# Kernel tuning notes

Measured on AMD Instinct MI355X. Metric: run time of the kernel, lower is better.

The kernel has to match this reference:

```python
import jax, jax.numpy as jnp
import numpy as np

B, N, P, T = 64, 200, 400, 1200
TOPK, STRIDE = 3, 25
THRESHOLD = 0.3  # args.threshold
EPS = 1e-9


def setup_inputs() -> dict:
    key = jax.random.key(0)
    k1, k2, k3 = jax.random.split(key, 3)
    x = jax.random.normal(k1, (B, N, T), jnp.float32)
    # xavier_uniform with gain=1.414 on (P, N) parameter
    limit = 1.414 * np.sqrt(6.0 / (P + N))
    patterns = jax.random.uniform(k2, (P, N), jnp.float32, -limit, limit)
    length = jax.random.randint(k3, (B,), 500, T + 1).astype(jnp.int32)
    return {"x": x, "patterns": patterns, "length": length}


def _forward(x, patterns, length):
    # size after temporal max-pool, per sample
    size_after_pool = jnp.floor(length.astype(jnp.float32) / STRIDE)  # (B,)

    # L2-normalize the learned patterns (P, N)
    normalized_patterns = patterns / jnp.sqrt((patterns ** 2).sum(-1, keepdims=True) + EPS)

    # top_select: keep top-K entries by |value| along node dim
    _, topi = jax.lax.top_k(jnp.abs(normalized_patterns), TOPK)  # (P, K)
    mask = jnp.zeros((P, N), jnp.float32).at[jnp.arange(P)[:, None], topi].set(1.0)
    toppattern = mask * normalized_patterns  # (P, N)

    # HCP_static branch: frames = x.transpose(2,1) -> (B, T, N)
    frames = x.transpose(0, 2, 1)
    normalized_frames = frames / jnp.sqrt((frames ** 2).sum(-1, keepdims=True) + EPS)

    # cosine similarity of every frame to every pattern: (B, T, P)
    sim = jnp.einsum('btn,pn->btp', normalized_frames, normalized_patterns)

    # non-overlapping max-pool over time with kernel=stride=STRIDE
    simw = sim.transpose(0, 2, 1).reshape(B, P, T // STRIDE, STRIDE)  # (B,P,Tp,S)
    posscores = simw.max(-1)          # (B, P, Tp)
    negscores = (-simw).max(-1)       # (B, P, Tp)
    sap = size_after_pool[:, None, None]
    compos = (posscores / sap).sum(-1)  # (B, P)
    comneg = (negscores / sap).sum(-1)  # (B, P)
    PES = (compos + comneg) / 2.0       # (B, P)

    # graphs = key_patterns.T @ diag(PES) @ key_patterns * non_diag_scale
    key_patterns = jax.lax.stop_gradient(toppattern)  # detach
    c = TOPK * P / N
    non_diag_scale = jnp.full((N, N), c, jnp.float32) - jnp.eye(N, dtype=jnp.float32) * (c - 1.0)
    graphs = jnp.einsum('pn,bp,pm->bnm', key_patterns, PES, key_patterns) * non_diag_scale

    # SigLoss(normalized_patterns, toppattern)
    lenp = jnp.linalg.norm(normalized_patterns, axis=-1)
    lentopp = jnp.linalg.norm(toppattern, axis=-1)
    norm = ((1.0 - lentopp / lenp) ** 2).mean()

    # Relaxed_orthloss(normalized_patterns, threshold)
    simpp = (normalized_patterns @ normalized_patterns.T) * (1.0 - jnp.eye(P, dtype=jnp.float32))
    orth = (jax.nn.relu((jnp.abs(simpp) - THRESHOLD) / (1.0 - THRESHOLD + 1e-5)) ** 2).mean()

    return graphs, norm, orth


def reference(x, patterns, length):
    return _forward(x, patterns, length)
```

## Files before the change

### kernel.cpp

```cpp
#include <hip/hip_runtime.h>
#include <math.h>

#define B_ 64
#define N_ 200
#define P_ 400
#define T_ 1200
#define TPAD 1280
#define PPAD 512
#define STRIDE_ 25
#define EPS_ 1e-9f
#define KPAD 224
#define BSTRIDE 232

#define OFF_NPATT  0
#define OFF_NPB16  80000
#define OFF_KEYVAL 124800
#define OFF_KEYIDX 126400
#define OFF_PES    128000
#define OFF_NORMB  153600
#define OFF_ORTHB  153700
#define OFF_NORM   OFF_NORMB
#define OFF_ORTH   OFF_ORTHB
#define OFF_NPBT   153728
#define OFF_XN     211072
#define OFF_GPOOL  9386112
#define WS_FAST_FLOATS (9386112 + 2457600)

#define ZO_BLKS  160
#define ZG_BLKS  40
#define ZP_BLKS  2
#define PAT_BLKS 100
#define TN_BLKS  (20 * B_)
#define Z_ALL    (ZO_BLKS + ZG_BLKS + ZP_BLKS)
#define PREP_BLKS (Z_ALL + PAT_BLKS + TN_BLKS)

typedef float f4v __attribute__((ext_vector_type(4)));
typedef short s8v __attribute__((ext_vector_type(8)));

__device__ inline unsigned short f2bf(float f) {
    union { float f; unsigned u; } v; v.f = f;
    unsigned r = v.u + 0x7FFFu + ((v.u >> 16) & 1u);
    return (unsigned short)(r >> 16);
}
__device__ inline unsigned okey(float f) {
    unsigned u = __float_as_uint(f);
    return (u & 0x80000000u) ? ~u : (u | 0x80000000u);
}
__device__ inline float dekey(unsigned k) {
    unsigned u = (k & 0x80000000u) ? (k & 0x7fffffffu) : ~k;
    return __uint_as_float(u);
}

__device__ float pat_body(const float* __restrict__ patterns, float* __restrict__ ws,
                          int p, int lane) {
    float v0 = patterns[p * N_ + lane];
    float v1 = patterns[p * N_ + lane + 64];
    float v2 = patterns[p * N_ + lane + 128];
    float v3 = (lane < 8) ? patterns[p * N_ + lane + 192] : 0.0f;

    float ss = v0 * v0 + v1 * v1 + v2 * v2 + v3 * v3;
    for (int off = 32; off; off >>= 1) ss += __shfl_down(ss, off);
    ss = __shfl(ss, 0);

    float rn = 1.0f / sqrtf(ss + EPS_);
    float s0 = v0 * rn, s1 = v1 * rn, s2 = v2 * rn, s3 = v3 * rn;

    float* npatT = ws + OFF_NPATT;
    npatT[(lane) * P_ + p] = s0;
    npatT[(lane + 64) * P_ + p] = s1;
    npatT[(lane + 128) * P_ + p] = s2;
    if (lane < 8) npatT[(lane + 192) * P_ + p] = s3;

    unsigned short* npb = (unsigned short*)(ws + OFF_NPB16);
    unsigned short b0 = f2bf(s0), b1 = f2bf(s1), b2 = f2bf(s2), b3 = f2bf(s3);
    npb[p * KPAD + lane] = b0;
    npb[p * KPAD + lane + 64] = b1;
    npb[p * KPAD + lane + 128] = b2;
    if (lane < 8) npb[p * KPAD + lane + 192] = b3;
    if (lane < 24) npb[p * KPAD + 200 + lane] = 0;

    unsigned short* npbT = (unsigned short*)(ws + OFF_NPBT);
    {
        int k0 = lane, k1 = lane + 64, k2 = lane + 128;
        npbT[(k0 >> 3) * (PPAD * 8) + p * 8 + (k0 & 7)] = b0;
        npbT[(k1 >> 3) * (PPAD * 8) + p * 8 + (k1 & 7)] = b1;
        npbT[(k2 >> 3) * (PPAD * 8) + p * 8 + (k2 & 7)] = b2;
        if (lane < 8) {
            int k3 = lane + 192;
            npbT[(k3 >> 3) * (PPAD * 8) + p * 8 + (k3 & 7)] = b3;
        }
        if (lane < 24) {
            int k4 = 200 + lane;
            npbT[(k4 >> 3) * (PPAD * 8) + p * 8 + (k4 & 7)] = 0;
        }
    }

    float a0 = fabsf(s0), a1 = fabsf(s1), a2 = fabsf(s2), a3 = fabsf(s3);

    int ch0 = -1, ch1 = -1, ch2 = -1;
    float cs0 = 0.f, cs1 = 0.f, cs2 = 0.f;

    for (int r = 0; r < 3; r++) {
        float bv = -1.0f;
        int bi = 1 << 30;
        {
            int n = lane;
            bool sk = (n == ch0) || (n == ch1) || (n == ch2);
            if (!sk && a0 > bv) { bv = a0; bi = n; }
        }
        {
            int n = lane + 64;
            bool sk = (n == ch0) || (n == ch1) || (n == ch2);
            if (!sk && (a1 > bv || (a1 == bv && n < bi))) { bv = a1; bi = n; }
        }
        {
            int n = lane + 128;
            bool sk = (n == ch0) || (n == ch1) || (n == ch2);
            if (!sk && (a2 > bv || (a2 == bv && n < bi))) { bv = a2; bi = n; }
        }
        if (lane < 8) {
            int n = lane + 192;
            bool sk = (n == ch0) || (n == ch1) || (n == ch2);
            if (!sk && (a3 > bv || (a3 == bv && n < bi))) { bv = a3; bi = n; }
        }
        for (int off = 32; off; off >>= 1) {
            float ov = __shfl_down(bv, off);
            int oi = __shfl_down(bi, off);
            if (ov > bv || (ov == bv && oi < bi)) { bv = ov; bi = oi; }
        }
        bi = __shfl(bi, 0);
        int slot = bi >> 6, src = bi & 63;
        float mine = (slot == 0) ? s0 : (slot == 1) ? s1 : (slot == 2) ? s2 : s3;
        float sval = __shfl(mine, src);
        if (r == 0) { ch0 = bi; cs0 = sval; }
        else if (r == 1) { ch1 = bi; cs1 = sval; }
        else { ch2 = bi; cs2 = sval; }
    }

    float d2 = 0.f;
    if (lane == 0) {
        float* keyval = ws + OFF_KEYVAL;
        int* keyidx = (int*)(ws + OFF_KEYIDX);
        keyval[p * 4 + 0] = cs0; keyval[p * 4 + 1] = cs1; keyval[p * 4 + 2] = cs2;
        keyidx[p * 4 + 0] = ch0; keyidx[p * 4 + 1] = ch1; keyidx[p * 4 + 2] = ch2;
        float lenp = sqrtf(ss) * rn;
        float lentopp = sqrtf(cs0 * cs0 + cs1 * cs1 + cs2 * cs2);
        float d = 1.0f - lentopp / lenp;
        d2 = d * d * (1.0f / (float)P_);
    }
    return d2;
}

__global__ __launch_bounds__(256) void prep_kernel(const float* __restrict__ x,
                                                   const float* __restrict__ patterns,
                                                   float* __restrict__ ws,
                                                   float* __restrict__ out) {
    __shared__ unsigned short xt16[64 * 210];
    __shared__ float psums[256];
    __shared__ float rns[64];
    __shared__ float sh4[4];

    const int tid = threadIdx.x;

    if (blockIdx.x < Z_ALL) {
        int zb = blockIdx.x;
        if (zb < ZO_BLKS) {
            uint4* o4 = (uint4*)out;
            for (int i = zb * 256 + tid; i < 640000; i += ZO_BLKS * 256)
                o4[i] = make_uint4(0, 0, 0, 0);
        } else if (zb < ZO_BLKS + ZG_BLKS) {
            uint4* gp4 = (uint4*)(ws + OFF_GPOOL);
            int base = (zb - ZO_BLKS) * 15360 + tid;
#pragma unroll
            for (int i = 0; i < 60; ++i)
                gp4[base + i * 256] = make_uint4(0, 0, 0, 0);
        } else {
            unsigned* p32 = (unsigned*)(ws + OFF_NPBT);
            int lb = zb - ZO_BLKS - ZG_BLKS;
            for (int e = lb * 256 + tid; e < 12544; e += ZP_BLKS * 256) {
                int seg = e / 448, r32 = e % 448;
                p32[seg * 2048 + 1600 + r32] = 0u;
            }
        }
        return;
    }

    if (blockIdx.x < Z_ALL + PAT_BLKS) {
        int pblk = blockIdx.x - Z_ALL;
        int wv = tid >> 6, lane = tid & 63;
        int p = pblk * 4 + wv;
        float d2 = pat_body(patterns, ws, p, lane);
        if (lane == 0) sh4[wv] = d2;
        __syncthreads();
        if (tid == 0)
            ws[OFF_NORMB + pblk] = sh4[0] + sh4[1] + sh4[2] + sh4[3];
        return;
    }

    const int blk = blockIdx.x - Z_ALL - PAT_BLKS;
    const int t = tid & 63, r = tid >> 6;
    const int b = blk / 20;
    const int t0 = (blk % 20) * 64;
    const bool valid = (t0 + t) < T_;

    float ss = 0.0f;
    if (valid) {
        const float* xp = x + (size_t)b * N_ * T_ + t0 + t;
#pragma unroll 5
        for (int i = 0; i < 50; ++i) {
            int n = r * 50 + i;
            float v = xp[(size_t)n * T_];
            ss += v * v;
            xt16[t * 210 + n] = f2bf(v);
        }
    }
    psums[tid] = ss;
    __syncthreads();
    if (tid < 64) {
        float s = psums[tid] + psums[tid + 64] + psums[tid + 128] + psums[tid + 192];
        rns[tid] = rsqrtf(s + EPS_);
    }
    __syncthreads();

    unsigned short* xnT = (unsigned short*)(ws + OFF_XN);
#pragma unroll
    for (int j = 0; j < 7; ++j) {
        int idx = tid + 256 * j;
        int seg = idx >> 6, tt = idx & 63;
        s8v ov = (s8v){0, 0, 0, 0, 0, 0, 0, 0};
        if (seg < 25 && (t0 + tt) < T_) {
            float rn = rns[tt];
            const unsigned* src = (const unsigned*)&xt16[tt * 210 + seg * 8];
            unsigned o[4];
#pragma unroll
            for (int i = 0; i < 4; ++i) {
                unsigned u = src[i];
                float lo = __uint_as_float(u << 16) * rn;
                float hi = __uint_as_float(u & 0xffff0000u) * rn;
                o[i] = (unsigned)f2bf(lo) | ((unsigned)f2bf(hi) << 16);
            }
            ov = (s8v){(short)(o[0] & 0xffff), (short)(o[0] >> 16),
                       (short)(o[1] & 0xffff), (short)(o[1] >> 16),
                       (short)(o[2] & 0xffff), (short)(o[2] >> 16),
                       (short)(o[3] & 0xffff), (short)(o[3] >> 16)};
        }
        *(s8v*)(xnT + (((size_t)b * 28 + seg) * TPAD + t0 + tt) * 8) = ov;
    }
}

__global__ __launch_bounds__(256, 4) void work_kernel(float* __restrict__ ws,
                                                      unsigned* __restrict__ gpool) {
    __shared__ short ldsB[80 * BSTRIDE];
    __shared__ unsigned pool[2 * 7 * 80];

    const int tid = threadIdx.x;
    int orig = blockIdx.x;
    int xcd = orig & 7, rem = orig >> 3;
    int nid = (xcd < 4 ? xcd * 83 : 4 * 83 + (xcd - 4) * 82) + rem;

    const bool isOrth = (nid >= 640);
    int pb, mbg, b;
    if (isOrth) { int o = nid - 640; pb = o % 5; mbg = o / 5; b = 0; }
    else        { pb = nid % 5; mbg = (nid / 5) % 2; b = nid / 10; }

    const unsigned short* npb = (const unsigned short*)(ws + OFF_NPB16) + (size_t)(pb * 80) * KPAD;

#pragma unroll
    for (int j = 0; j < 9; ++j) {
        int idx = tid + 256 * j;
        if (idx < 2240) {
            int row = idx / 28, seg = idx % 28;
            *(s8v*)(&ldsB[row * BSTRIDE + seg * 8]) = *(const s8v*)(npb + (size_t)row * KPAD + seg * 8);
        }
    }
    for (int i = tid; i < 1120; i += 256) pool[i] = 0u;
    __syncthreads();

    const int wv = tid >> 6;
    const int lane = tid & 63;
    const int l15 = lane & 15, kg = lane >> 4;

    const int ROWS = isOrth ? PPAD : TPAD;
    const unsigned short* abase = isOrth
        ? (const unsigned short*)(ws + OFF_NPBT)
        : (const unsigned short*)(ws + OFF_XN) + (size_t)b * 28 * TPAD * 8;
    const int segstep = 4 * ROWS * 8;
    const int niter = isOrth ? 1 : 5;

    float orthpart = 0.f;

    for (int it = 0; it < niter; ++it) {
        const int mb = isOrth ? mbg : (mbg * 5 + it);
        const int row0 = mb * 128 + wv * 32 + l15;
        const unsigned short* ar0 = abase + ((size_t)kg * ROWS + row0) * 8;
        const unsigned short* ar1 = ar0 + 16 * 8;

        f4v acc[2][5];
#pragma unroll
        for (int mi = 0; mi < 2; ++mi)
#pragma unroll
            for (int ni = 0; ni < 5; ++ni) acc[mi][ni] = (f4v){0.f, 0.f, 0.f, 0.f};

        s8v A[4][2];
#pragma unroll
        for (int c = 0; c < 4; ++c) {
            A[c][0] = *(const s8v*)(ar0 + c * segstep);
            A[c][1] = *(const s8v*)(ar1 + c * segstep);
        }

#pragma unroll
        for (int c = 0; c < 7; ++c) {
            if (c + 4 < 7) {
                A[(c + 4) & 3][0] = *(const s8v*)(ar0 + (c + 4) * segstep);
                A[(c + 4) & 3][1] = *(const s8v*)(ar1 + (c + 4) * segstep);
            }
            s8v bf[5];
#pragma unroll
            for (int ni = 0; ni < 5; ++ni)
                bf[ni] = *(const s8v*)(&ldsB[(ni * 16 + l15) * BSTRIDE + c * 32 + kg * 8]);
#pragma unroll
            for (int ni = 0; ni < 5; ++ni) {
                acc[0][ni] = __builtin_amdgcn_mfma_f32_16x16x32_bf16(A[c & 3][0], bf[ni], acc[0][ni], 0, 0, 0);
                acc[1][ni] = __builtin_amdgcn_mfma_f32_16x16x32_bf16(A[c & 3][1], bf[ni], acc[1][ni], 0, 0, 0);
            }
        }

        if (isOrth) {
#pragma unroll
            for (int mi = 0; mi < 2; ++mi) {
                int rb = mb * 128 + wv * 32 + mi * 16 + kg * 4;
#pragma unroll
                for (int ni = 0; ni < 5; ++ni) {
                    int col = pb * 80 + ni * 16 + l15;
#pragma unroll
                    for (int jj = 0; jj < 4; ++jj) {
                        if (rb + jj == col) continue;
                        float t = (fabsf(acc[mi][ni][jj]) - 0.3f) * (1.0f / 0.70001f);
                        if (t > 0.0f) orthpart += t * t;
                    }
                }
            }
            break;
        }

        const int wbase = (mb * 128) / 25;
#pragma unroll
        for (int mi = 0; mi < 2; ++mi) {
            int f0 = mb * 128 + wv * 32 + mi * 16 + kg * 4;
            int w0 = f0 / 25, w3 = (f0 + 3) / 25;
            int wsplit = w3 * 25;
#pragma unroll
            for (int ni = 0; ni < 5; ++ni) {
                int pc = ni * 16 + l15;
                float p0 = -1e30f, p1 = -1e30f, n0 = -1e30f, n1 = -1e30f;
#pragma unroll
                for (int jj = 0; jj < 4; ++jj) {
                    float v = acc[mi][ni][jj];
                    if (f0 + jj < wsplit) { p0 = fmaxf(p0, v); n0 = fmaxf(n0, -v); }
                    else                 { p1 = fmaxf(p1, v); n1 = fmaxf(n1, -v); }
                }
                atomicMax(&pool[(0 * 7 + (w3 - wbase)) * 80 + pc], okey(p1));
                atomicMax(&pool[(1 * 7 + (w3 - wbase)) * 80 + pc], okey(n1));
                if (w0 != w3) {
                    atomicMax(&pool[(0 * 7 + (w0 - wbase)) * 80 + pc], okey(p0));
                    atomicMax(&pool[(1 * 7 + (w0 - wbase)) * 80 + pc], okey(n0));
                }
            }
        }
        __syncthreads();
        for (int e = tid; e < 1120; e += 256) {
            unsigned v = pool[e];
            pool[e] = 0u;
            if (!v) continue;
            int pass = e / 560, r2 = e % 560;
            int w = wbase + r2 / 80, p = r2 % 80;
            if (w < 48)
                atomicMax(&gpool[((size_t)(pass * B_ + b) * 48 + w) * 400 + pb * 80 + p], v);
        }
        __syncthreads();
    }

    if (isOrth) {
        for (int off = 32; off; off >>= 1) orthpart += __shfl_down(orthpart, off);
        __syncthreads();
        float* red = (float*)pool;
        if (lane == 0) red[wv] = orthpart;
        __syncthreads();
        if (tid == 0)
            ws[OFF_ORTHB + (nid - 640)] = (red[0] + red[1] + red[2] + red[3]) *
                                          (1.0f / ((float)P_ * (float)P_));
    }
}

__global__ __launch_bounds__(256) void graphs_kernel(const unsigned* __restrict__ gpool,
                                                     const int* __restrict__ length,
                                                     const float* __restrict__ ws,
                                                     float* __restrict__ out) {
    int idx = blockIdx.x * 256 + threadIdx.x;
    if (idx == 0) {
        float sn = 0.f;
        for (int i = 0; i < PAT_BLKS; ++i) sn += ws[OFF_NORMB + i];
        out[(size_t)B_ * N_ * N_] = sn;
        float so = 0.f;
        for (int i = 0; i < 20; ++i) so += ws[OFF_ORTHB + i];
        out[(size_t)B_ * N_ * N_ + 1] = so;
    }
    if (idx >= B_ * P_) return;
    int b = idx / P_;
    int p = idx - b * P_;

    const unsigned* gp0 = gpool + (size_t)b * 48 * 400 + p;
    const unsigned* gp1 = gpool + (size_t)(B_ + b) * 48 * 400 + p;
    float s = 0.f;
#pragma unroll
    for (int w = 0; w < 48; ++w)
        s += dekey(gp0[w * 400]) + dekey(gp1[w * 400]);
    float rsap = 1.0f / (float)(length[b] / STRIDE_);
    float e = s * 0.5f * rsap;

    const float* keyval = ws + OFF_KEYVAL;
    const int* keyidx = (const int*)(ws + OFF_KEYIDX);
    float va[3] = { keyval[p * 4 + 0], keyval[p * 4 + 1], keyval[p * 4 + 2] };
    int ia[3] = { keyidx[p * 4 + 0], keyidx[p * 4 + 1], keyidx[p * 4 + 2] };

    float* g = out + (size_t)b * N_ * N_;
#pragma unroll
    for (int a = 0; a < 3; a++) {
#pragma unroll
        for (int c = 0; c < 3; c++) {
            float scale = (ia[a] == ia[c]) ? 1.0f : 6.0f;
            atomicAdd(&g[ia[a] * N_ + ia[c]], va[a] * va[c] * e * scale);
        }
    }
}

__global__ __launch_bounds__(256) void main_kernel(const float* __restrict__ x,
                                                   const int* __restrict__ length,
                                                   const float* __restrict__ ws,
                                                   float* __restrict__ pes) {
    __shared__ float xs[N_][STRIDE_ + 1];
    __shared__ float rnorm[STRIDE_];
    __shared__ float poolp[P_][5];
    __shared__ float pooln[P_][5];

    int w = blockIdx.x;
    int b = blockIdx.y;
    const float* xb = x + (size_t)b * N_ * T_ + (size_t)w * STRIDE_;

    for (int i = threadIdx.x; i < N_ * STRIDE_; i += 256) {
        int n = i / STRIDE_;
        int t = i - n * STRIDE_;
        xs[n][t] = xb[n * T_ + t];
    }
    __syncthreads();

    if (threadIdx.x < STRIDE_) {
        float ssf = 0.0f;
        for (int n = 0; n < N_; n++) { float vv = xs[n][threadIdx.x]; ssf += vv * vv; }
        rnorm[threadIdx.x] = 1.0f / sqrtf(ssf + EPS_);
    }
    __syncthreads();

    int pt = threadIdx.x % 50;
    int tt = threadIdx.x / 50;

    if (tt < 5) {
        float acc[8][5];
#pragma unroll
        for (int i = 0; i < 8; i++)
#pragma unroll
            for (int j = 0; j < 5; j++) acc[i][j] = 0.0f;

        const float4* np4 = (const float4*)(ws + OFF_NPATT);
        int pbq = pt * 2;
        for (int n = 0; n < N_; n++) {
            float4 q0 = np4[n * (P_ / 4) + pbq];
            float4 q1 = np4[n * (P_ / 4) + pbq + 1];
            float qa[8] = { q0.x, q0.y, q0.z, q0.w, q1.x, q1.y, q1.z, q1.w };
            float xv0 = xs[n][tt * 5 + 0];
            float xv1 = xs[n][tt * 5 + 1];
            float xv2 = xs[n][tt * 5 + 2];
            float xv3 = xs[n][tt * 5 + 3];
            float xv4 = xs[n][tt * 5 + 4];
#pragma unroll
            for (int i = 0; i < 8; i++) {
                acc[i][0] += qa[i] * xv0;
                acc[i][1] += qa[i] * xv1;
                acc[i][2] += qa[i] * xv2;
                acc[i][3] += qa[i] * xv3;
                acc[i][4] += qa[i] * xv4;
            }
        }
#pragma unroll
        for (int i = 0; i < 8; i++) {
            float pm = -1e30f, nm = -1e30f;
#pragma unroll
            for (int j = 0; j < 5; j++) {
                float s = acc[i][j] * rnorm[tt * 5 + j];
                pm = fmaxf(pm, s);
                nm = fmaxf(nm, -s);
            }
            poolp[pt * 8 + i][tt] = pm;
            pooln[pt * 8 + i][tt] = nm;
        }
    }
    __syncthreads();

    float rsap = 1.0f / (float)(length[b] / STRIDE_);
    for (int p = threadIdx.x; p < P_; p += 256) {
        float pm = poolp[p][0], nm = pooln[p][0];
#pragma unroll
        for (int q = 1; q < 5; q++) {
            pm = fmaxf(pm, poolp[p][q]);
            nm = fmaxf(nm, pooln[p][q]);
        }
        atomicAdd(&pes[b * P_ + p], (pm + nm) * 0.5f * rsap);
    }
}

__global__ __launch_bounds__(256) void fb_graphs_kernel(const float* __restrict__ ws,
                                                        float* __restrict__ out) {
    int idx = blockIdx.x * 256 + threadIdx.x;
    if (idx == 0) {
        out[(size_t)B_ * N_ * N_] = ws[OFF_NORM];
        out[(size_t)B_ * N_ * N_ + 1] = ws[OFF_ORTH];
    }
    if (idx >= B_ * P_) return;
    int b = idx / P_;
    int p = idx - b * P_;
    float e = ws[OFF_PES + b * P_ + p];
    const float* keyval = ws + OFF_KEYVAL;
    const int* keyidx = (const int*)(ws + OFF_KEYIDX);
    float va[3] = { keyval[p * 4 + 0], keyval[p * 4 + 1], keyval[p * 4 + 2] };
    int ia[3] = { keyidx[p * 4 + 0], keyidx[p * 4 + 1], keyidx[p * 4 + 2] };
    float* g = out + (size_t)b * N_ * N_;
#pragma unroll
    for (int a = 0; a < 3; a++)
#pragma unroll
        for (int c = 0; c < 3; c++) {
            float scale = (ia[a] == ia[c]) ? 1.0f : 6.0f;
            atomicAdd(&g[ia[a] * N_ + ia[c]], va[a] * va[c] * e * scale);
        }
}

__global__ __launch_bounds__(64) void pat_kernel(const float* __restrict__ patterns,
                                                 float* __restrict__ ws) {
    float d2 = pat_body(patterns, ws, blockIdx.x, threadIdx.x & 63);
    if (threadIdx.x == 0) atomicAdd(ws + OFF_NORM, d2);
}
__global__ __launch_bounds__(256) void orth_kernel(float* __restrict__ ws) {
    __shared__ float rowi[N_];
    __shared__ float red[256];
    const float* npatT = ws + OFF_NPATT;
    int i = blockIdx.x;
    for (int k = threadIdx.x; k < N_; k += 256) rowi[k] = npatT[k * P_ + i];
    __syncthreads();
    float partial = 0.0f;
    for (int j = threadIdx.x; j < P_; j += 256) {
        if (j == i) continue;
        float s = 0.0f;
        for (int k = 0; k < N_; k++) s += rowi[k] * npatT[k * P_ + j];
        float t = (fabsf(s) - 0.3f) * (1.0f / 0.70001f);
        if (t > 0.0f) partial += t * t;
    }
    red[threadIdx.x] = partial;
    __syncthreads();
    for (int sft = 128; sft; sft >>= 1) {
        if (threadIdx.x < sft) red[threadIdx.x] += red[threadIdx.x + sft];
        __syncthreads();
    }
    if (threadIdx.x == 0)
        atomicAdd(ws + OFF_ORTH, red[0] * (1.0f / ((float)P_ * (float)P_)));
}

extern "C" void kernel_launch(void* const* d_in, const int* in_sizes, int n_in,
                              void* d_out, int out_size, void* d_ws, size_t ws_size,
                              hipStream_t stream) {
    const float* x = (const float*)d_in[0];
    const float* patterns = (const float*)d_in[1];
    const int* length = (const int*)d_in[2];
    float* out = (float*)d_out;
    float* ws = (float*)d_ws;

    if (ws_size >= (size_t)WS_FAST_FLOATS * sizeof(float)) {
        unsigned* gpool = (unsigned*)(ws + OFF_GPOOL);
        prep_kernel<<<PREP_BLKS, 256, 0, stream>>>(x, patterns, ws, out);
        work_kernel<<<660, 256, 0, stream>>>(ws, gpool);
        graphs_kernel<<<(B_ * P_ + 255) / 256, 256, 0, stream>>>(gpool, length, ws, out);
    } else {
        hipMemsetAsync(d_out, 0, (size_t)B_ * N_ * N_ * sizeof(float), stream);
        hipMemsetAsync(ws + OFF_PES, 0, (size_t)(B_ * P_) * sizeof(float), stream);
        hipMemsetAsync(ws + OFF_NORM, 0, sizeof(float), stream);
        hipMemsetAsync(ws + OFF_ORTH, 0, sizeof(float), stream);
        pat_kernel<<<P_, 64, 0, stream>>>(patterns, ws);
        orth_kernel<<<P_, 256, 0, stream>>>(ws);
        main_kernel<<<dim3(T_ / STRIDE_, B_), 256, 0, stream>>>(x, length, ws, ws + OFF_PES);
        fb_graphs_kernel<<<(B_ * P_ + 255) / 256, 256, 0, stream>>>(ws, out);
    }
}
```

Measured before the change: 75.53 us.

## Build graph rows in shared memory instead of zeroing output and global atomics

Removes the 10 MB output zero-fill from the prep kernel and replaces global atomicAdd scatter into the graphs with a new kernel. Each block owns 8 rows of one sample's graph, accumulates contributions in shared memory, and writes the rows with plain vector stores. PES values are now computed in a separate small kernel and stored to workspace. This adds an extra kernel launch, and each row block scans all 400 patterns.

```diff
diff --git a/kernel.cpp b/kernel.cpp
--- a/kernel.cpp
+++ b/kernel.cpp
@@ -26,12 +26,11 @@
 #define OFF_GPOOL  9386112
 #define WS_FAST_FLOATS (9386112 + 2457600)
 
-#define ZO_BLKS  160
 #define ZG_BLKS  40
 #define ZP_BLKS  2
 #define PAT_BLKS 100
 #define TN_BLKS  (20 * B_)
-#define Z_ALL    (ZO_BLKS + ZG_BLKS + ZP_BLKS)
+#define Z_ALL    (ZG_BLKS + ZP_BLKS)
 #define PREP_BLKS (Z_ALL + PAT_BLKS + TN_BLKS)
 
 typedef float f4v __attribute__((ext_vector_type(4)));
@@ -142,7 +141,9 @@
         float* keyval = ws + OFF_KEYVAL;
         int* keyidx = (int*)(ws + OFF_KEYIDX);
         keyval[p * 4 + 0] = cs0; keyval[p * 4 + 1] = cs1; keyval[p * 4 + 2] = cs2;
+        keyval[p * 4 + 3] = 0.f;
         keyidx[p * 4 + 0] = ch0; keyidx[p * 4 + 1] = ch1; keyidx[p * 4 + 2] = ch2;
+        keyidx[p * 4 + 3] = -1;
         float lenp = sqrtf(ss) * rn;
         float lentopp = sqrtf(cs0 * cs0 + cs1 * cs1 + cs2 * cs2);
         float d = 1.0f - lentopp / lenp;
@@ -153,8 +154,7 @@
 
 __global__ __launch_bounds__(256) void prep_kernel(const float* __restrict__ x,
                                                    const float* __restrict__ patterns,
-                                                   float* __restrict__ ws,
-                                                   float* __restrict__ out) {
+                                                   float* __restrict__ ws) {
     __shared__ unsigned short xt16[64 * 210];
     __shared__ float psums[256];
     __shared__ float rns[64];
@@ -164,19 +164,15 @@
 
     if (blockIdx.x < Z_ALL) {
         int zb = blockIdx.x;
-        if (zb < ZO_BLKS) {
-            uint4* o4 = (uint4*)out;
-            for (int i = zb * 256 + tid; i < 640000; i += ZO_BLKS * 256)
-                o4[i] = make_uint4(0, 0, 0, 0);
-        } else if (zb < ZO_BLKS + ZG_BLKS) {
+        if (zb < ZG_BLKS) {
             uint4* gp4 = (uint4*)(ws + OFF_GPOOL);
-            int base = (zb - ZO_BLKS) * 15360 + tid;
+            int base = zb * 15360 + tid;
 #pragma unroll
             for (int i = 0; i < 60; ++i)
                 gp4[base + i * 256] = make_uint4(0, 0, 0, 0);
         } else {
             unsigned* p32 = (unsigned*)(ws + OFF_NPBT);
-            int lb = zb - ZO_BLKS - ZG_BLKS;
+            int lb = zb - ZG_BLKS;
             for (int e = lb * 256 + tid; e < 12544; e += ZP_BLKS * 256) {
                 int seg = e / 448, r32 = e % 448;
                 p32[seg * 2048 + 1600 + r32] = 0u;
@@ -392,23 +388,13 @@
     }
 }
 
-__global__ __launch_bounds__(256) void graphs_kernel(const unsigned* __restrict__ gpool,
-                                                     const int* __restrict__ length,
-                                                     const float* __restrict__ ws,
-                                                     float* __restrict__ out) {
+__global__ __launch_bounds__(256) void pes_kernel(const unsigned* __restrict__ gpool,
+                                                  const int* __restrict__ length,
+                                                  float* __restrict__ ws) {
     int idx = blockIdx.x * 256 + threadIdx.x;
-    if (idx == 0) {
-        float sn = 0.f;
-        for (int i = 0; i < PAT_BLKS; ++i) sn += ws[OFF_NORMB + i];
-        out[(size_t)B_ * N_ * N_] = sn;
-        float so = 0.f;
-        for (int i = 0; i < 20; ++i) so += ws[OFF_ORTHB + i];
-        out[(size_t)B_ * N_ * N_ + 1] = so;
-    }
     if (idx >= B_ * P_) return;
     int b = idx / P_;
     int p = idx - b * P_;
-
     const unsigned* gp0 = gpool + (size_t)b * 48 * 400 + p;
     const unsigned* gp1 = gpool + (size_t)(B_ + b) * 48 * 400 + p;
     float s = 0.f;
@@ -416,21 +402,55 @@
     for (int w = 0; w < 48; ++w)
         s += dekey(gp0[w * 400]) + dekey(gp1[w * 400]);
     float rsap = 1.0f / (float)(length[b] / STRIDE_);
-    float e = s * 0.5f * rsap;
-
-    const float* keyval = ws + OFF_KEYVAL;
-    const int* keyidx = (const int*)(ws + OFF_KEYIDX);
-    float va[3] = { keyval[p * 4 + 0], keyval[p * 4 + 1], keyval[p * 4 + 2] };
-    int ia[3] = { keyidx[p * 4 + 0], keyidx[p * 4 + 1], keyidx[p * 4 + 2] };
-
-    float* g = out + (size_t)b * N_ * N_;
-#pragma unroll
-    for (int a = 0; a < 3; a++) {
-#pragma unroll
-        for (int c = 0; c < 3; c++) {
-            float scale = (ia[a] == ia[c]) ? 1.0f : 6.0f;
-            atomicAdd(&g[ia[a] * N_ + ia[c]], va[a] * va[c] * e * scale);
-        }
+    ws[OFF_PES + b * P_ + p] = s * 0.5f * rsap;
+}
+
+__global__ __launch_bounds__(256) void graphs_row_kernel(const float* __restrict__ ws,
+                                                         float* __restrict__ out) {
+    __shared__ float rowbuf[8 * 200];
+    __shared__ int   ki[400][4];
+    __shared__ float kv[400][4];
+    __shared__ float el[400];
+
+    const int tid = threadIdx.x;
+    const int b = blockIdx.x / 25;
+    const int n0 = (blockIdx.x % 25) * 8;
+
+    for (int i = tid; i < 1600; i += 256) rowbuf[i] = 0.f;
+    for (int p = tid; p < 400; p += 256) {
+        *(int4*)ki[p] = ((const int4*)(ws + OFF_KEYIDX))[p];
+        *(float4*)kv[p] = ((const float4*)(ws + OFF_KEYVAL))[p];
+        el[p] = ws[OFF_PES + b * P_ + p];
+    }
+    __syncthreads();
+
+    for (int p = tid; p < 400; p += 256) {
+        float e = el[p];
+#pragma unroll
+        for (int a = 0; a < 3; ++a) {
+            int n = ki[p][a];
+            if (n < n0 || n >= n0 + 8) continue;
+            float va = kv[p][a] * e;
+#pragma unroll
+            for (int c = 0; c < 3; ++c) {
+                float scale = (a == c) ? 1.0f : 6.0f;
+                atomicAdd(&rowbuf[(n - n0) * 200 + ki[p][c]], va * kv[p][c] * scale);
+            }
+        }
+    }
+    __syncthreads();
+
+    float4* dst = (float4*)(out + (size_t)b * N_ * N_ + (size_t)n0 * N_);
+    const float4* srcb = (const float4*)rowbuf;
+    for (int i = tid; i < 400; i += 256) dst[i] = srcb[i];
+
+    if (blockIdx.x == 0 && tid == 0) {
+        float sn = 0.f;
+        for (int i = 0; i < PAT_BLKS; ++i) sn += ws[OFF_NORMB + i];
+        float so = 0.f;
+        for (int i = 0; i < 20; ++i) so += ws[OFF_ORTHB + i];
+        out[(size_t)B_ * N_ * N_] = sn;
+        out[(size_t)B_ * N_ * N_ + 1] = so;
     }
 }
 
@@ -584,9 +604,10 @@
 
     if (ws_size >= (size_t)WS_FAST_FLOATS * sizeof(float)) {
         unsigned* gpool = (unsigned*)(ws + OFF_GPOOL);
-        prep_kernel<<<PREP_BLKS, 256, 0, stream>>>(x, patterns, ws, out);
+        prep_kernel<<<PREP_BLKS, 256, 0, stream>>>(x, patterns, ws);
         work_kernel<<<660, 256, 0, stream>>>(ws, gpool);
-        graphs_kernel<<<(B_ * P_ + 255) / 256, 256, 0, stream>>>(gpool, length, ws, out);
+        pes_kernel<<<(B_ * P_ + 255) / 256, 256, 0, stream>>>(gpool, length, ws);
+        graphs_row_kernel<<<B_ * 25, 256, 0, stream>>>(ws, out);
     } else {
         hipMemsetAsync(d_out, 0, (size_t)B_ * N_ * N_ * sizeof(float), stream);
         hipMemsetAsync(ws + OFF_PES, 0, (size_t)(B_ * P_) * sizeof(float), stream);
```

Measured after the change: 68.18 us. 9.7% less time.
